# Kernel optimization log

Hardware: AMD Instinct MI355X
Metric: run time of the kernel (lower is better)

## Reference

```python
import jax, jax.numpy as jnp
import numpy as np

MAX_DISP = 4  # matches init_kwargs max_displacement


def setup_inputs() -> dict:
    key = jax.random.key(0)
    k1, k2 = jax.random.split(key)
    B, C, H, W = 8, 512, 64, 128
    f1 = jax.random.normal(k1, (B, C, H, W), dtype=jnp.float32)
    f2 = jax.random.normal(k2, (B, C, H, W), dtype=jnp.float32)
    return {"f1": f1, "f2": f2}


def reference(f1, f2):
    # Windowed cross-correlation with circular (torch.roll) boundary handling.
    # For each displacement (dy, dx) in [-MAX_DISP, MAX_DISP]^2, shift f2
    # circularly along (H, W) and reduce over channels.
    # Output: [B, (2*MAX_DISP+1)**2, H, W], displacement order = row-major (dy, dx),
    # matching the original nested loop / torch.cat order.
    outs = [
        jnp.sum(f1 * jnp.roll(f2, (dy, dx), axis=(2, 3)), axis=1)  # [B, H, W]
        for dy in range(-MAX_DISP, MAX_DISP + 1)
        for dx in range(-MAX_DISP, MAX_DISP + 1)
    ]
    return jnp.stack(outs, axis=1)  # [B, 81, H, W]
```

## Files before the change

### kernel.cpp

```cpp
#include <hip/hip_runtime.h>
#include <hip/hip_bf16.h>


typedef short  bf16x8  __attribute__((ext_vector_type(8)));
typedef short  short4v __attribute__((ext_vector_type(4)));
typedef float  f32x4   __attribute__((ext_vector_type(4)));

#define NB 8
#define NC 512
#define NH 64
#define NW 128
#define HW (NH * NW)
#define TH 16
#define TW 16
#define CC 64
#define NSTAGE (NC / CC)
#define LROW 24
#define LCP  72
#define LDS_SHORTS (LROW * 2 * 16 * LCP)

__device__ __forceinline__ short f2bf(float x) {
  union { __hip_bfloat16 h; short s; } u;
  u.h = __float2bfloat16(x);
  return u.s;
}

__global__ __launch_bounds__(512, 2)
void corr_mfma(const float* __restrict__ f1, const float* __restrict__ f2,
               float* __restrict__ out) {
  __shared__ short lds[LDS_SHORTS];

  const int t    = threadIdx.x;
  const int b    = blockIdx.x & 7;
  const int tile = blockIdx.x >> 3;
  const int h0   = (tile >> 3) * TH;
  const int w0   = (tile & 7) * TW;

  const int wv = t >> 6;
  const int l  = t & 63;
  const int lg = l >> 4;
  const int lw = l & 15;

  const int sw  = t & 15;
  const int scq = (t >> 4) & 7;
  const int srb = t >> 7;

  const float* f1b = f1 + b * NC * HW;
  const float* f2b = f2 + b * NC * HW;

  f32x4 acc[2][9][2];
#pragma unroll
  for (int hh = 0; hh < 2; ++hh)
#pragma unroll
    for (int d = 0; d < 9; ++d)
#pragma unroll
      for (int wt = 0; wt < 2; ++wt)
        acc[hh][d][wt] = (f32x4){0.f, 0.f, 0.f, 0.f};

  const int hA = h0 + 2 * wv;

  for (int st = 0; st < NSTAGE; ++st) {
    const int c0 = st * CC;

    float a_raw[2][2][8];
#pragma unroll
    for (int kk = 0; kk < 2; ++kk)
#pragma unroll
      for (int hh = 0; hh < 2; ++hh) {
        const float* s = f1b + (c0 + kk * 32 + 8 * lg) * HW + (hA + hh) * NW + (w0 + lw);
#pragma unroll
        for (int e = 0; e < 8; ++e)
          a_raw[kk][hh][e] = s[e * HW];
      }

    __syncthreads();

#pragma unroll
    for (int wt = 0; wt < 2; ++wt) {
      const int wg = (w0 + wt * 16 - 4 + sw) & (NW - 1);
#pragma unroll
      for (int rr = 0; rr < 6; ++rr) {
        const int row = rr * 4 + srb;
        const int h2  = (h0 - 4 + row) & (NH - 1);
        const float* src = f2b + c0 * HW + h2 * NW + wg;
        short* dst = lds + (row * 2 + wt) * (16 * LCP) + sw * LCP;
#pragma unroll
        for (int cc = 0; cc < 2; ++cc) {
          const int cb = scq * 4 + cc * 32;
          float x0 = src[(cb + 0) * HW];
          float x1 = src[(cb + 1) * HW];
          float x2 = src[(cb + 2) * HW];
          float x3 = src[(cb + 3) * HW];
          short4v v = { f2bf(x0), f2bf(x1), f2bf(x2), f2bf(x3) };
          *reinterpret_cast<short4v*>(dst + cb) = v;
        }
      }
    }

    bf16x8 afr[2][2];
#pragma unroll
    for (int kk = 0; kk < 2; ++kk)
#pragma unroll
      for (int hh = 0; hh < 2; ++hh)
#pragma unroll
        for (int e = 0; e < 8; ++e)
          afr[kk][hh][e] = f2bf(a_raw[kk][hh][e]);

    __syncthreads();

#pragma unroll
    for (int kk = 0; kk < 2; ++kk) {
#pragma unroll
      for (int ro = 0; ro < 10; ++ro) {
        const int row = 2 * wv + ro;
#pragma unroll
        for (int wt = 0; wt < 2; ++wt) {
          const bf16x8 bfr = *reinterpret_cast<const bf16x8*>(
              lds + (row * 2 + wt) * (16 * LCP) + lw * LCP + kk * 32 + 8 * lg);
          if (ro <= 8)
            acc[0][8 - ro][wt] = __builtin_amdgcn_mfma_f32_16x16x32_bf16(
                afr[kk][0], bfr, acc[0][8 - ro][wt], 0, 0, 0);
          if (ro >= 1)
            acc[1][9 - ro][wt] = __builtin_amdgcn_mfma_f32_16x16x32_bf16(
                afr[kk][1], bfr, acc[1][9 - ro][wt], 0, 0, 0);
        }
      }
    }
  }

#pragma unroll
  for (int hh = 0; hh < 2; ++hh) {
    const int h = hA + hh;
#pragma unroll
    for (int d = 0; d < 9; ++d) {
#pragma unroll
      for (int wt = 0; wt < 2; ++wt) {
#pragma unroll
        for (int r = 0; r < 4; ++r) {
          const int p   = 4 * lg + r;
          const int dxi = p - lw + (wt == 0 ? 8 : -8);
          if (dxi >= 0 && dxi <= 8) {
            out[((b * 81 + d * 9 + dxi) * NH + h) * NW + (w0 + p)] = acc[hh][d][wt][r];
          }
        }
      }
    }
  }
}

extern "C" void kernel_launch(void* const* d_in, const int* in_sizes, int n_in,
                              void* d_out, int out_size, void* d_ws, size_t ws_size,
                              hipStream_t stream) {
  const float* f1 = (const float*)d_in[0];
  const float* f2 = (const float*)d_in[1];
  float* out = (float*)d_out;
  corr_mfma<<<dim3(256), dim3(512), 0, stream>>>(f1, f2, out);
}
```

Measured before the change: 317.5 us.

## Double-buffer LDS stages with smaller tiles and more blocks

Halves the tile height to 8 rows and the channel chunk to 32, and launches 512 blocks of 256 threads instead of 256 blocks of 512. LDS is double-buffered so the next stage's f1 registers and f2 tile are loaded while MFMAs run on the current buffer, leaving one barrier per stage. The aim is to hide global-load latency and improve occupancy across CUs. In exchange there are twice as many stages and barriers, and the halo rows are reloaded relatively more often with smaller tiles.

After: 347.8 us. 9.5% more time.

```diff
diff --git a/kernel.cpp b/kernel.cpp
--- a/kernel.cpp
+++ b/kernel.cpp
@@ -6,18 +6,17 @@
 typedef short  short4v __attribute__((ext_vector_type(4)));
 typedef float  f32x4   __attribute__((ext_vector_type(4)));
 
-#define NB 8
 #define NC 512
 #define NH 64
 #define NW 128
 #define HW (NH * NW)
-#define TH 16
+#define TH 8
 #define TW 16
-#define CC 64
-#define NSTAGE (NC / CC)
-#define LROW 24
-#define LCP  72
-#define LDS_SHORTS (LROW * 2 * 16 * LCP)
+#define CC 32
+#define NST (NC / CC)
+#define LROW 16
+#define LCP 40
+#define BUFS (LROW * 32 * LCP)
 
 __device__ __forceinline__ short f2bf(float x) {
   union { __hip_bfloat16 h; short s; } u;
@@ -25,10 +24,10 @@
   return u.s;
 }
 
-__global__ __launch_bounds__(512, 2)
+__global__ __launch_bounds__(256, 2)
 void corr_mfma(const float* __restrict__ f1, const float* __restrict__ f2,
                float* __restrict__ out) {
-  __shared__ short lds[LDS_SHORTS];
+  __shared__ short lds[2 * BUFS];
 
   const int t    = threadIdx.x;
   const int b    = blockIdx.x & 7;
@@ -41,9 +40,9 @@
   const int lg = l >> 4;
   const int lw = l & 15;
 
-  const int sw  = t & 15;
-  const int scq = (t >> 4) & 7;
-  const int srb = t >> 7;
+  const int sw  = t & 31;
+  const int scq = t >> 5;
+  const int wg  = (w0 - 4 + sw) & (NW - 1);
 
   const float* f1b = f1 + b * NC * HW;
   const float* f2b = f2 + b * NC * HW;
@@ -59,73 +58,75 @@
 
   const int hA = h0 + 2 * wv;
 
-  for (int st = 0; st < NSTAGE; ++st) {
-    const int c0 = st * CC;
-
-    float a_raw[2][2][8];
-#pragma unroll
-    for (int kk = 0; kk < 2; ++kk)
-#pragma unroll
-      for (int hh = 0; hh < 2; ++hh) {
-        const float* s = f1b + (c0 + kk * 32 + 8 * lg) * HW + (hA + hh) * NW + (w0 + lw);
-#pragma unroll
-        for (int e = 0; e < 8; ++e)
-          a_raw[kk][hh][e] = s[e * HW];
-      }
-
-    __syncthreads();
+  float a_nxt[2][8];
 
 #pragma unroll
-    for (int wt = 0; wt < 2; ++wt) {
-      const int wg = (w0 + wt * 16 - 4 + sw) & (NW - 1);
+  for (int hh = 0; hh < 2; ++hh) {
+    const float* s = f1b + (8 * lg) * HW + (hA + hh) * NW + (w0 + lw);
 #pragma unroll
-      for (int rr = 0; rr < 6; ++rr) {
-        const int row = rr * 4 + srb;
-        const int h2  = (h0 - 4 + row) & (NH - 1);
-        const float* src = f2b + c0 * HW + h2 * NW + wg;
-        short* dst = lds + (row * 2 + wt) * (16 * LCP) + sw * LCP;
+    for (int e = 0; e < 8; ++e) a_nxt[hh][e] = s[e * HW];
+  }
+  {
+    const float* src = f2b + (4 * scq) * HW + wg;
+    short* dst = lds + sw * LCP + 4 * scq;
 #pragma unroll
-        for (int cc = 0; cc < 2; ++cc) {
-          const int cb = scq * 4 + cc * 32;
-          float x0 = src[(cb + 0) * HW];
-          float x1 = src[(cb + 1) * HW];
-          float x2 = src[(cb + 2) * HW];
-          float x3 = src[(cb + 3) * HW];
-          short4v v = { f2bf(x0), f2bf(x1), f2bf(x2), f2bf(x3) };
-          *reinterpret_cast<short4v*>(dst + cb) = v;
-        }
+    for (int r = 0; r < LROW; ++r) {
+      const int h2 = (h0 - 4 + r) & (NH - 1);
+      const float* s = src + h2 * NW;
+      float x0 = s[0], x1 = s[HW], x2 = s[2 * HW], x3 = s[3 * HW];
+      short4v v = { f2bf(x0), f2bf(x1), f2bf(x2), f2bf(x3) };
+      *reinterpret_cast<short4v*>(dst + r * 32 * LCP) = v;
+    }
+  }
+  __syncthreads();
+
+  for (int st = 0; st < NST; ++st) {
+    const int cur = st & 1;
+
+    bf16x8 afr[2];
+#pragma unroll
+    for (int hh = 0; hh < 2; ++hh)
+#pragma unroll
+      for (int e = 0; e < 8; ++e)
+        afr[hh][e] = f2bf(a_nxt[hh][e]);
+
+    const short* bbase = lds + cur * BUFS;
+#pragma unroll
+    for (int ro = 0; ro < 10; ++ro) {
+      const int row = 2 * wv + ro;
+#pragma unroll
+      for (int wt = 0; wt < 2; ++wt) {
+        const bf16x8 bfr = *reinterpret_cast<const bf16x8*>(
+            bbase + (row * 32 + 16 * wt + lw) * LCP + 8 * lg);
+        if (ro <= 8)
+          acc[0][8 - ro][wt] = __builtin_amdgcn_mfma_f32_16x16x32_bf16(
+              afr[0], bfr, acc[0][8 - ro][wt], 0, 0, 0);
+        if (ro >= 1)
+          acc[1][9 - ro][wt] = __builtin_amdgcn_mfma_f32_16x16x32_bf16(
+              afr[1], bfr, acc[1][9 - ro][wt], 0, 0, 0);
       }
     }
 
-    bf16x8 afr[2][2];
+    if (st + 1 < NST) {
+      const int c0 = (st + 1) * CC;
 #pragma unroll
-    for (int kk = 0; kk < 2; ++kk)
+      for (int hh = 0; hh < 2; ++hh) {
+        const float* s = f1b + (c0 + 8 * lg) * HW + (hA + hh) * NW + (w0 + lw);
 #pragma unroll
-      for (int hh = 0; hh < 2; ++hh)
+        for (int e = 0; e < 8; ++e) a_nxt[hh][e] = s[e * HW];
+      }
+      const float* src = f2b + (c0 + 4 * scq) * HW + wg;
+      short* dst = lds + (1 - cur) * BUFS + sw * LCP + 4 * scq;
 #pragma unroll
-        for (int e = 0; e < 8; ++e)
-          afr[kk][hh][e] = f2bf(a_raw[kk][hh][e]);
-
-    __syncthreads();
-
-#pragma unroll
-    for (int kk = 0; kk < 2; ++kk) {
-#pragma unroll
-      for (int ro = 0; ro < 10; ++ro) {
-        const int row = 2 * wv + ro;
-#pragma unroll
-        for (int wt = 0; wt < 2; ++wt) {
-          const bf16x8 bfr = *reinterpret_cast<const bf16x8*>(
-              lds + (row * 2 + wt) * (16 * LCP) + lw * LCP + kk * 32 + 8 * lg);
-          if (ro <= 8)
-            acc[0][8 - ro][wt] = __builtin_amdgcn_mfma_f32_16x16x32_bf16(
-                afr[kk][0], bfr, acc[0][8 - ro][wt], 0, 0, 0);
-          if (ro >= 1)
-            acc[1][9 - ro][wt] = __builtin_amdgcn_mfma_f32_16x16x32_bf16(
-                afr[kk][1], bfr, acc[1][9 - ro][wt], 0, 0, 0);
-        }
+      for (int r = 0; r < LROW; ++r) {
+        const int h2 = (h0 - 4 + r) & (NH - 1);
+        const float* s = src + h2 * NW;
+        float x0 = s[0], x1 = s[HW], x2 = s[2 * HW], x3 = s[3 * HW];
+        short4v v = { f2bf(x0), f2bf(x1), f2bf(x2), f2bf(x3) };
+        *reinterpret_cast<short4v*>(dst + r * 32 * LCP) = v;
       }
     }
+    __syncthreads();
   }
 
 #pragma unroll
@@ -154,5 +155,5 @@
   const float* f1 = (const float*)d_in[0];
   const float* f2 = (const float*)d_in[1];
   float* out = (float*)d_out;
-  corr_mfma<<<dim3(256), dim3(512), 0, stream>>>(f1, f2, out);
+  corr_mfma<<<dim3(512), dim3(256), 0, stream>>>(f1, f2, out);
 }
```
